# Kernel optimization log

Measured on AMD Instinct MI355X. Metric: run time of the kernel, lower is better.

## Reference

```python
import jax, jax.numpy as jnp
import numpy as np

N_QUBITS = 10   # log2(32*32)
N_LAYERS = 5
GRID = 32


def _u3_gates(weights):
    # weights: [L, Q, 3] float32 -> gates: [L, Q, 2, 2] complex64
    th, ph, lm = weights[..., 0], weights[..., 1], weights[..., 2]
    cos = jnp.cos(th / 2)
    sin = jnp.sin(th / 2)
    u00 = cos.astype(jnp.complex64)
    u01 = -jnp.exp(1j * lm) * sin
    u10 = jnp.exp(1j * ph) * sin
    u11 = jnp.exp(1j * (ph + lm)) * cos
    row0 = jnp.stack([u00, u01], axis=-1)
    row1 = jnp.stack([u10, u11], axis=-1)
    return jnp.stack([row0, row1], axis=-2)


def _build_unitary(weights):
    N = 1 << N_QUBITS
    gates = _u3_gates(weights)
    # U as tensor [N, 2, 2, ..., 2]; axis q+1 is qubit q's column index
    U = jnp.eye(N, dtype=jnp.complex64).reshape((N,) + (2,) * N_QUBITS)
    for l in range(N_LAYERS):
        # single-qubit U3 rotations
        for q in range(N_QUBITS):
            ax = q + 1
            s = jnp.moveaxis(U, ax, -1)
            s = jnp.einsum('...a,ba->...b', s, gates[l, q])
            U = jnp.moveaxis(s, -1, ax)
        # circular CNOTs: control q -> target (q+1) % N_QUBITS
        for q in range(N_QUBITS):
            c_ax = q + 1
            t_ax = ((q + 1) % N_QUBITS) + 1
            s = jnp.moveaxis(U, (c_ax, t_ax), (-2, -1))
            # when control bit == 1, flip target bit (swap the two target slices)
            s = s.at[..., 1, :].set(s[..., 1, ::-1])
            U = jnp.moveaxis(s, (-2, -1), (c_ax, t_ax))
    return U.reshape(N, N)


def setup_inputs() -> dict:
    key = jax.random.key(0)
    k1, k2 = jax.random.split(key)
    x_freq = jax.random.normal(k1, (128, 16, GRID, GRID), dtype=jnp.float32)
    weights = jax.random.normal(k2, (N_LAYERS, N_QUBITS, 3), dtype=jnp.float32) * 0.1
    return {"x_freq": x_freq, "weights": weights}


def reference(x_freq, weights):
    B, C, H, W = x_freq.shape
    state = x_freq.reshape(B, C, -1).astype(jnp.complex64)  # [B, C, N]
    U = _build_unitary(weights)                              # [N, N]
    out = jnp.einsum('ij,bcj->bci', U, state)
    return out.reshape(B, C, H, W)
```

## Files before the change

kernel.cpp:

```cpp
#include <hip/hip_runtime.h>


#define NQ 10
#define NL 5
#define NST 1024
#define NTH 64
#define SV_STRIDE 1028

constexpr int csigma(int i) {
  for (int q = 0; q < NQ; ++q) {
    const int cb = 9 - q, tb = 9 - ((q + 1) % NQ);
    i ^= ((i >> cb) & 1) << tb;
  }
  return i;
}

__device__ __forceinline__ int swz(int k) { return k ^ (((k >> 5) & 15) << 1); }

__global__ void build_gates(const float* __restrict__ w, float* __restrict__ gw) {
  const int t = threadIdx.x;
  if (t < NL * NQ) {
    const float th = w[t * 3 + 0], ph = w[t * 3 + 1], lm = w[t * 3 + 2];
    const float ch = cosf(0.5f * th), sh = sinf(0.5f * th);
    const float cl = cosf(lm), sl = sinf(lm);
    const float cp = cosf(ph), sp = sinf(ph);
    const float cpl = cosf(ph + lm), spl = sinf(ph + lm);
    float* G = gw + t * 8;
    G[0] = ch;       G[1] = 0.0f;
    G[2] = cp * sh;  G[3] = sp * sh;
    G[4] = -cl * sh; G[5] = -sl * sh;
    G[6] = cpl * ch; G[7] = spl * ch;
  }
}

__device__ __forceinline__ void bfly(float2& a, float2& b, const float h00,
                                     const float2 h01, const float2 h10,
                                     const float2 h11) {
  const float nar = h00 * a.x + h01.x * b.x - h01.y * b.y;
  const float nai = h00 * a.y + h01.x * b.y + h01.y * b.x;
  const float nbr = h10.x * a.x - h10.y * a.y + h11.x * b.x - h11.y * b.y;
  const float nbi = h10.x * a.y + h10.y * a.x + h11.x * b.y + h11.y * b.x;
  a = make_float2(nar, nai);
  b = make_float2(nbr, nbi);
}

__global__ __launch_bounds__(NTH) void qc_apply(
    const float* __restrict__ x, const float* __restrict__ gw,
    float* __restrict__ out, int out_size) {
  __shared__ float2 sc[2 * SV_STRIDE];

  const int t = threadIdx.x;
  const int lane = t & 31;
  const int svLocal = t >> 5;
  const int svGlobal = blockIdx.x * 2 + svLocal;
  const int svo = svLocal * SV_STRIDE;
  float4* const s4 = (float4*)(sc + svo);

  {
    const float* xs = x + (size_t)svGlobal * NST;
#pragma unroll
    for (int r = 0; r < 8; ++r) {
      const int k = lane * 4 + 128 * r;
      const float4 xv = *(const float4*)(xs + k);
      const int p01 = swz(k);
      const int p23 = p01 ^ 2;
      *(float4*)&sc[svo + p01] = make_float4(xv.x, 0.f, xv.y, 0.f);
      *(float4*)&sc[svo + p23] = make_float4(xv.z, 0.f, xv.w, 0.f);
    }
  }
  __syncthreads();

  int sL = lane;
#pragma unroll
  for (int q = 0; q < NQ; ++q) {
    const int cb = 9 - q, tb = 9 - ((q + 1) % NQ);
    sL ^= ((sL >> cb) & 1) << tb;
  }
  constexpr int SH0 = csigma(1 << 5), SH1 = csigma(1 << 6),
                SH2 = csigma(1 << 7), SH3 = csigma(1 << 8),
                SH4 = csigma(1 << 9);

  const int m = (lane & 15) << 1;
  float2 w2[32];

#pragma unroll 1
  for (int l = NL - 1; l >= 0; --l) {
    const float* gl = gw + l * NQ * 8;

    float2 v[32];
#pragma unroll
    for (int j = 0; j < 32; ++j) {
      const int idx = sL ^ ((j & 1) ? SH0 : 0) ^ ((j & 2) ? SH1 : 0) ^
                      ((j & 4) ? SH2 : 0) ^ ((j & 8) ? SH3 : 0) ^
                      ((j & 16) ? SH4 : 0);
      v[j] = sc[svo + swz(idx)];
    }
#pragma unroll
    for (int e = 0; e < 5; ++e) {
      const float* G = gl + (4 - e) * 8;
      const float h00 = G[0];
      const float2 h01 = make_float2(G[2], G[3]);
      const float2 h10 = make_float2(G[4], G[5]);
      const float2 h11 = make_float2(G[6], G[7]);
#pragma unroll
      for (int j = 0; j < 32; ++j)
        if (!(j & (1 << e))) bfly(v[j], v[j | (1 << e)], h00, h01, h10, h11);
    }
    __syncthreads();
#pragma unroll
    for (int j = 0; j < 32; ++j)
      sc[svo + swz((j << 5) | lane)] = v[j];
    __syncthreads();

#pragma unroll
    for (int a = 0; a < 16; ++a) {
      const float4 p = s4[((lane << 5) + ((2 * a) ^ m)) >> 1];
      w2[2 * a]     = make_float2(p.x, p.y);
      w2[2 * a + 1] = make_float2(p.z, p.w);
    }
#pragma unroll
    for (int e = 0; e < 5; ++e) {
      const float* G = gl + (9 - e) * 8;
      const float h00 = G[0];
      const float2 h01 = make_float2(G[2], G[3]);
      const float2 h10 = make_float2(G[4], G[5]);
      const float2 h11 = make_float2(G[6], G[7]);
#pragma unroll
      for (int i = 0; i < 32; ++i)
        if (!(i & (1 << e))) bfly(w2[i], w2[i | (1 << e)], h00, h01, h10, h11);
    }
    if (l != 0) {
#pragma unroll
      for (int a = 0; a < 16; ++a)
        s4[((lane << 5) + ((2 * a) ^ m)) >> 1] =
            make_float4(w2[2 * a].x, w2[2 * a].y, w2[2 * a + 1].x, w2[2 * a + 1].y);
      __syncthreads();
    }
  }

  const size_t ob = (size_t)svGlobal * NST + (lane << 5);
#pragma unroll
  for (int a = 0; a < 8; ++a) {
    if (ob + 4 * a + 4 <= (size_t)out_size)
      *(float4*)(out + ob + 4 * a) =
          make_float4(w2[4 * a].x, w2[4 * a + 1].x, w2[4 * a + 2].x, w2[4 * a + 3].x);
  }
}

extern "C" void kernel_launch(void* const* d_in, const int* in_sizes, int n_in,
                              void* d_out, int out_size, void* d_ws, size_t ws_size,
                              hipStream_t stream) {
  const float* x = (const float*)d_in[0];
  const float* w = (const float*)d_in[1];
  float* out = (float*)d_out;
  float* gw = (float*)d_ws;
  const int nstates = in_sizes[0] / NST;
  build_gates<<<1, 64, 0, stream>>>(w, gw);
  qc_apply<<<nstates / 2, NTH, 0, stream>>>(x, gw, out, out_size);
}
```

Measured before the change: 93.52 us.

## Split each statevector across 64 threads with three-pass butterfly schedule

Each block now handles one 1024-amplitude statevector with 64 threads holding 16 amplitudes each, instead of two statevectors with 32 threads holding 32 each. Qubit butterflies are regrouped into 4+2+4 passes through shared memory with a new swizzle, and the complex butterfly uses 2-wide vector types. The goal is to cut per-thread register use, raise occupancy and launch twice as many blocks. The cost is an extra shared-memory round trip and two more barriers per layer.

```diff
diff --git a/kernel.cpp b/kernel.cpp
--- a/kernel.cpp
+++ b/kernel.cpp
@@ -5,7 +5,8 @@
 #define NL 5
 #define NST 1024
 #define NTH 64
-#define SV_STRIDE 1028
+
+typedef float f2 __attribute__((ext_vector_type(2)));
 
 constexpr int csigma(int i) {
   for (int q = 0; q < NQ; ++q) {
@@ -15,7 +16,7 @@
   return i;
 }
 
-__device__ __forceinline__ int swz(int k) { return k ^ (((k >> 5) & 15) << 1); }
+__device__ __forceinline__ int swz(int k) { return k ^ (((k >> 4) & 7) << 1); }
 
 __global__ void build_gates(const float* __restrict__ w, float* __restrict__ gw) {
   const int t = threadIdx.x;
@@ -33,117 +34,127 @@
   }
 }
 
-__device__ __forceinline__ void bfly(float2& a, float2& b, const float h00,
-                                     const float2 h01, const float2 h10,
-                                     const float2 h11) {
-  const float nar = h00 * a.x + h01.x * b.x - h01.y * b.y;
-  const float nai = h00 * a.y + h01.x * b.y + h01.y * b.x;
-  const float nbr = h10.x * a.x - h10.y * a.y + h11.x * b.x - h11.y * b.y;
-  const float nbi = h10.x * a.y + h10.y * a.x + h11.x * b.y + h11.y * b.x;
-  a = make_float2(nar, nai);
-  b = make_float2(nbr, nbi);
+__device__ __forceinline__ void bfly(f2& a, f2& b, const float h00,
+                                     const float h01x, const float h01y,
+                                     const float h10x, const float h10y,
+                                     const float h11x, const float h11y) {
+  const f2 ia = (f2){-a.y, a.x};
+  const f2 ib = (f2){-b.y, b.x};
+  const f2 na = h00 * a + h01x * b + h01y * ib;
+  const f2 nb = h10x * a + h10y * ia + h11x * b + h11y * ib;
+  a = na;
+  b = nb;
 }
+
+#define LOAD_G(G)                                             \
+  const float h00 = (G)[0];                                   \
+  const float h01x = (G)[2], h01y = (G)[3];                   \
+  const float h10x = (G)[4], h10y = (G)[5];                   \
+  const float h11x = (G)[6], h11y = (G)[7];
 
 __global__ __launch_bounds__(NTH) void qc_apply(
     const float* __restrict__ x, const float* __restrict__ gw,
     float* __restrict__ out, int out_size) {
-  __shared__ float2 sc[2 * SV_STRIDE];
+  __shared__ alignas(16) f2 sc[NST];
 
   const int t = threadIdx.x;
-  const int lane = t & 31;
-  const int svLocal = t >> 5;
-  const int svGlobal = blockIdx.x * 2 + svLocal;
-  const int svo = svLocal * SV_STRIDE;
-  float4* const s4 = (float4*)(sc + svo);
+  const int sv = blockIdx.x;
+  const int m = (t & 7) << 1;
 
   {
-    const float* xs = x + (size_t)svGlobal * NST;
+    const float* xs = x + (size_t)sv * NST;
 #pragma unroll
-    for (int r = 0; r < 8; ++r) {
-      const int k = lane * 4 + 128 * r;
-      const float4 xv = *(const float4*)(xs + k);
-      const int p01 = swz(k);
-      const int p23 = p01 ^ 2;
-      *(float4*)&sc[svo + p01] = make_float4(xv.x, 0.f, xv.y, 0.f);
-      *(float4*)&sc[svo + p23] = make_float4(xv.z, 0.f, xv.w, 0.f);
+    for (int jp = 0; jp < 4; ++jp) {
+      const float4 xv = ((const float4*)xs)[t * 4 + jp];
+      const int j0 = (jp * 4) ^ m;
+      *(float4*)&sc[(t << 4) | j0]       = make_float4(xv.x, 0.f, xv.y, 0.f);
+      *(float4*)&sc[(t << 4) | (j0 ^ 2)] = make_float4(xv.z, 0.f, xv.w, 0.f);
     }
   }
   __syncthreads();
 
-  int sL = lane;
+  int sL = t;
 #pragma unroll
   for (int q = 0; q < NQ; ++q) {
     const int cb = 9 - q, tb = 9 - ((q + 1) % NQ);
     sL ^= ((sL >> cb) & 1) << tb;
   }
-  constexpr int SH0 = csigma(1 << 5), SH1 = csigma(1 << 6),
-                SH2 = csigma(1 << 7), SH3 = csigma(1 << 8),
-                SH4 = csigma(1 << 9);
+  constexpr int SH6 = csigma(1 << 6), SH7 = csigma(1 << 7),
+                SH8 = csigma(1 << 8), SH9 = csigma(1 << 9);
 
-  const int m = (lane & 15) << 1;
-  float2 w2[32];
+  f2 v[16];
 
 #pragma unroll 1
   for (int l = NL - 1; l >= 0; --l) {
     const float* gl = gw + l * NQ * 8;
 
-    float2 v[32];
 #pragma unroll
-    for (int j = 0; j < 32; ++j) {
-      const int idx = sL ^ ((j & 1) ? SH0 : 0) ^ ((j & 2) ? SH1 : 0) ^
-                      ((j & 4) ? SH2 : 0) ^ ((j & 8) ? SH3 : 0) ^
-                      ((j & 16) ? SH4 : 0);
-      v[j] = sc[svo + swz(idx)];
+    for (int r = 0; r < 16; ++r) {
+      const int idx = sL ^ ((r & 1) ? SH6 : 0) ^ ((r & 2) ? SH7 : 0) ^
+                      ((r & 4) ? SH8 : 0) ^ ((r & 8) ? SH9 : 0);
+      v[r] = sc[swz(idx)];
     }
 #pragma unroll
-    for (int e = 0; e < 5; ++e) {
-      const float* G = gl + (4 - e) * 8;
-      const float h00 = G[0];
-      const float2 h01 = make_float2(G[2], G[3]);
-      const float2 h10 = make_float2(G[4], G[5]);
-      const float2 h11 = make_float2(G[6], G[7]);
+    for (int e = 0; e < 4; ++e) {
+      LOAD_G(gl + (3 - e) * 8)
 #pragma unroll
-      for (int j = 0; j < 32; ++j)
-        if (!(j & (1 << e))) bfly(v[j], v[j | (1 << e)], h00, h01, h10, h11);
+      for (int r = 0; r < 16; ++r)
+        if (!(r & (1 << e)))
+          bfly(v[r], v[r | (1 << e)], h00, h01x, h01y, h10x, h10y, h11x, h11y);
     }
     __syncthreads();
 #pragma unroll
-    for (int j = 0; j < 32; ++j)
-      sc[svo + swz((j << 5) | lane)] = v[j];
+    for (int r = 0; r < 16; ++r) sc[swz((r << 6) | t)] = v[r];
+    __syncthreads();
+
+    const int cbase = ((t >> 4) << 8) | (t & 15);
+#pragma unroll
+    for (int r = 0; r < 16; ++r) v[r] = sc[swz(cbase | (r << 4))];
+#pragma unroll
+    for (int e = 0; e < 2; ++e) {
+      LOAD_G(gl + (5 - e) * 8)
+#pragma unroll
+      for (int r = 0; r < 16; ++r)
+        if (!(r & (1 << e)))
+          bfly(v[r], v[r | (1 << e)], h00, h01x, h01y, h10x, h10y, h11x, h11y);
+    }
+    __syncthreads();
+#pragma unroll
+    for (int r = 0; r < 16; ++r) sc[swz(cbase | (r << 4))] = v[r];
     __syncthreads();
 
 #pragma unroll
-    for (int a = 0; a < 16; ++a) {
-      const float4 p = s4[((lane << 5) + ((2 * a) ^ m)) >> 1];
-      w2[2 * a]     = make_float2(p.x, p.y);
-      w2[2 * a + 1] = make_float2(p.z, p.w);
+    for (int rp = 0; rp < 8; ++rp) {
+      const float4 p = *(const float4*)&sc[(t << 4) | ((2 * rp) ^ m)];
+      v[2 * rp]     = (f2){p.x, p.y};
+      v[2 * rp + 1] = (f2){p.z, p.w};
     }
 #pragma unroll
-    for (int e = 0; e < 5; ++e) {
-      const float* G = gl + (9 - e) * 8;
-      const float h00 = G[0];
-      const float2 h01 = make_float2(G[2], G[3]);
-      const float2 h10 = make_float2(G[4], G[5]);
-      const float2 h11 = make_float2(G[6], G[7]);
+    for (int e = 0; e < 4; ++e) {
+      LOAD_G(gl + (9 - e) * 8)
 #pragma unroll
-      for (int i = 0; i < 32; ++i)
-        if (!(i & (1 << e))) bfly(w2[i], w2[i | (1 << e)], h00, h01, h10, h11);
+      for (int r = 0; r < 16; ++r)
+        if (!(r & (1 << e)))
+          bfly(v[r], v[r | (1 << e)], h00, h01x, h01y, h10x, h10y, h11x, h11y);
     }
     if (l != 0) {
 #pragma unroll
-      for (int a = 0; a < 16; ++a)
-        s4[((lane << 5) + ((2 * a) ^ m)) >> 1] =
-            make_float4(w2[2 * a].x, w2[2 * a].y, w2[2 * a + 1].x, w2[2 * a + 1].y);
+      for (int rp = 0; rp < 8; ++rp) {
+        *(float4*)&sc[(t << 4) | ((2 * rp) ^ m)] =
+            make_float4(v[2 * rp].x, v[2 * rp].y,
+                        v[2 * rp + 1].x, v[2 * rp + 1].y);
+      }
       __syncthreads();
     }
   }
 
-  const size_t ob = (size_t)svGlobal * NST + (lane << 5);
+  const size_t ob = (size_t)sv * NST + (t << 4);
 #pragma unroll
-  for (int a = 0; a < 8; ++a) {
-    if (ob + 4 * a + 4 <= (size_t)out_size)
-      *(float4*)(out + ob + 4 * a) =
-          make_float4(w2[4 * a].x, w2[4 * a + 1].x, w2[4 * a + 2].x, w2[4 * a + 3].x);
+  for (int rp = 0; rp < 4; ++rp) {
+    if (ob + 4 * rp + 4 <= (size_t)out_size)
+      *(float4*)(out + ob + 4 * rp) =
+          make_float4(v[4 * rp].x, v[4 * rp + 1].x,
+                      v[4 * rp + 2].x, v[4 * rp + 3].x);
   }
 }
 
@@ -156,5 +167,5 @@
   float* gw = (float*)d_ws;
   const int nstates = in_sizes[0] / NST;
   build_gates<<<1, 64, 0, stream>>>(w, gw);
-  qc_apply<<<nstates / 2, NTH, 0, stream>>>(x, gw, out, out_size);
+  qc_apply<<<nstates, NTH, 0, stream>>>(x, gw, out, out_size);
 }
```

Result: faster. 85.01 us (-9.1%).
